# Optimization experiments

Hardware: AMD Instinct MI355X
Metric: run time of the kernel (lower is better)

Reference implementation:

```python
import jax, jax.numpy as jnp
import numpy as np

N, E = 50000, 800000
IN_DIM, H0, H1, OUT_DIM = 64, 64, 64, 8
NUM_RELS, NUM_BASES = 16, 8


def setup_inputs() -> dict:
    key = jax.random.key(0)
    ks = jax.random.split(key, 20)
    features = jax.random.normal(ks[0], (N, IN_DIM), dtype=jnp.float32)
    etypes = jax.random.randint(ks[1], (E,), 0, NUM_RELS)
    src = jax.random.randint(ks[2], (E,), 0, N)
    dst = jax.random.randint(ks[3], (E,), 0, N)
    # degree normalization 1/in_degree(dst), as DGL stores in g.edata['norm']
    deg = jax.ops.segment_sum(jnp.ones((E,), jnp.float32), dst, num_segments=N)
    norm = (1.0 / jnp.maximum(deg, 1.0))[dst][:, None]  # [E,1]

    def glorot(k, shape):
        fan_in, fan_out = shape[-2], shape[-1]
        lim = jnp.sqrt(6.0 / (fan_in + fan_out)).astype(jnp.float32)
        return jax.random.uniform(k, shape, jnp.float32, -lim, lim)

    dims = [(IN_DIM, H0), (H0, H1), (H1, OUT_DIM)]
    inp = {"features": features, "norm": norm}
    for i, (di, do) in enumerate(dims):
        inp[f"basis{i}"] = glorot(ks[4 + 4 * i], (NUM_BASES, di, do))
        inp[f"comp{i}"] = glorot(ks[5 + 4 * i], (NUM_RELS, NUM_BASES))
        inp[f"loop{i}"] = glorot(ks[6 + 4 * i], (di, do))
        inp[f"bias{i}"] = jnp.zeros((do,), jnp.float32)
    inp["etypes"] = etypes
    inp["src"] = src
    inp["dst"] = dst
    return inp


def rel_graph_conv(h, basis, comp, loop_w, bias, etypes, src, dst, norm, act):
    # basis-decomposed relation weights: [R, din, dout]
    W = jnp.einsum('rb,bio->rio', comp, basis)
    # transform every node under every relation: [N, R, dout]
    h_trans = jnp.einsum('ni,rio->nro', h, W)
    # per-edge gather of (src node, edge relation), degree-normalized
    msg = h_trans[src, etypes] * norm  # [E, dout]
    agg = jax.ops.segment_sum(msg, dst, num_segments=h.shape[0])  # [N, dout]
    out = agg + h @ loop_w + bias  # self-loop + bias (DGL defaults)
    return act(out)


def reference(features, norm, basis0, comp0, loop0, bias0, basis1, comp1, loop1,
              bias1, basis2, comp2, loop2, bias2, etypes, src, dst):
    lrelu = lambda x: jax.nn.leaky_relu(x, negative_slope=0.01)
    h = rel_graph_conv(features, basis0, comp0, loop0, bias0, etypes, src, dst, norm, lrelu)
    h = rel_graph_conv(h, basis1, comp1, loop1, bias1, etypes, src, dst, norm, lrelu)
    h = rel_graph_conv(h, basis2, comp2, loop2, bias2, etypes, src, dst, norm, jax.nn.relu)
    return h
```

## Files before the change

kernel.cpp:

```cpp
#include <hip/hip_runtime.h>

#define NN 50000
#define NE 800000
#define CAP 64
#define KC 72
#define RNG 6250
#define EPB 2047

typedef __bf16 bf16x8 __attribute__((ext_vector_type(8)));
typedef float f32x4 __attribute__((ext_vector_type(4)));
typedef float f32x2 __attribute__((ext_vector_type(2)));
typedef unsigned short ushort;
typedef unsigned int uint;

__device__ inline ushort f2bf(float x) {
  uint u = __builtin_bit_cast(uint, x);
  u += 0x7FFF + ((u >> 16) & 1);
  return (ushort)(u >> 16);
}
__device__ inline float bf2f(ushort u) {
  return __builtin_bit_cast(float, (uint)u << 16);
}


__device__ inline void wprep_body(const float* __restrict__ basis,
                                  const float* __restrict__ loopw,
                                  ushort* __restrict__ W2, int DOUT, int NCOLS,
                                  int idx) {
  int total = KC * NCOLS * 8;
  if (idx >= total) return;
  int j = idx & 7;
  int n = (idx >> 3) % NCOLS;
  int kc = idx / (8 * NCOLS);
  int k = kc * 8 + j;
  float v = 0.f;
  if (n < DOUT) v = (k < 512) ? basis[k * DOUT + n] : loopw[(k - 512) * DOUT + n];
  W2[((size_t)kc * NCOLS + n) * 8 + j] = f2bf(v);
}

__global__ __launch_bounds__(256) void build_kernel(
    const int* __restrict__ dstv, const int* __restrict__ srcv,
    const int* __restrict__ etv, int* __restrict__ cursor, int* __restrict__ pk,
    const float* __restrict__ f, ushort* __restrict__ fb,
    const float* __restrict__ b0, const float* __restrict__ l0, ushort* __restrict__ W0,
    const float* __restrict__ b1, const float* __restrict__ l1, ushort* __restrict__ W1,
    const float* __restrict__ b2, const float* __restrict__ l2, ushort* __restrict__ W2,
    const float* __restrict__ c0, const float* __restrict__ c1,
    const float* __restrict__ c2, float* __restrict__ cp) {
  int blk = blockIdx.x;
  int tid = threadIdx.x;
  if (blk < 3128) {
    int sel = blk & 7;
    int sub = blk >> 3;
    int lo = sel * RNG;
    int start = sub * EPB;
    for (int t = tid; t < EPB; t += 256) {
      int i = start + t;
      if (i >= NE) break;
      int d = dstv[i];
      if ((uint)(d - lo) < (uint)RNG) {
        int p = atomicAdd(&cursor[d], 1);
        if (p < CAP) pk[d * CAP + p] = (etv[i] << 16) | srcv[i];
      }
    }
  } else if (blk < 6253) {
    int i = (blk - 3128) * 256 + tid;
    if (i < NN * 16) {
      float4 v = ((const float4*)f)[i];
      ushort4 u;
      u.x = f2bf(v.x); u.y = f2bf(v.y); u.z = f2bf(v.z); u.w = f2bf(v.w);
      ((ushort4*)fb)[i] = u;
    }
  } else if (blk < 6397) {
    wprep_body(b0, l0, W0, 64, 64, (blk - 6253) * 256 + tid);
  } else if (blk < 6541) {
    wprep_body(b1, l1, W1, 64, 64, (blk - 6397) * 256 + tid);
  } else if (blk < 6577) {
    wprep_body(b2, l2, W2, 8, 16, (blk - 6541) * 256 + tid);
  } else {
    int idx = (blk - 6577) * 256 + tid;
    if (idx < 408) {
      int l = idx / 136, k = idx % 136;
      const float* src = (l == 0) ? c0 : ((l == 1) ? c1 : c2);
      cp[idx] = (k < 128) ? src[k] : 0.f;
    }
  }
}


template <int DOUT, int NCOLS, bool OBF>
__global__ __launch_bounds__(1024, 8) void layer_kernel(
    const ushort* __restrict__ hb,
    const float* __restrict__ cpad,
    const int* __restrict__ degv,
    const int* __restrict__ pk,
    const ushort* __restrict__ W2,
    const float* __restrict__ bias,
    void* __restrict__ outp,
    float slope)
{
  __shared__ ushort X[KC][16][8];
  int tid = threadIdx.x;
  int wave = tid >> 6;
  int lane = tid & 63;
  int dbase = blockIdx.x * 16;
  int d = __builtin_amdgcn_readfirstlane(dbase + wave);

  int deg = degv[d];
  int dw = deg > CAP ? CAP : deg;
  const int4* p4 = (const int4*)(pk + (size_t)d * CAP);

  f32x2 acc2[4] = {{0.f, 0.f}, {0.f, 0.f}, {0.f, 0.f}, {0.f, 0.f}};
  for (int base = 0; base < dw; base += 8) {
    int qg = base >> 3;
    int4 e0 = p4[qg * 2];
    int4 e1 = p4[qg * 2 + 1];
    int pe[8] = {e0.x, e0.y, e0.z, e0.w, e1.x, e1.y, e1.z, e1.w};
    float hv[8];
    int ps[8];
#pragma unroll
    for (int i = 0; i < 8; ++i) {
      int pr = __builtin_amdgcn_readfirstlane(pe[i]);
      ps[i] = (base + i < dw) ? pr : (16 << 16);
      hv[i] = bf2f(hb[(size_t)(ps[i] & 0xFFFF) * 64 + lane]);
    }
#pragma unroll
    for (int i = 0; i < 8; ++i) {
      const f32x2* c2 = (const f32x2*)(cpad + (ps[i] >> 16) * 8);
      f32x2 h2 = {hv[i], hv[i]};
#pragma unroll
      for (int j = 0; j < 4; ++j)
        acc2[j] = __builtin_elementwise_fma(c2[j], h2, acc2[j]);
    }
  }

  float inv = 1.0f / (float)(deg > 1 ? deg : 1);
  int jj = lane & 7;
  int csub = lane >> 3;
#pragma unroll
  for (int b = 0; b < 8; ++b) {
    float v = ((b & 1) ? acc2[b >> 1].y : acc2[b >> 1].x) * inv;
    X[b * 8 + csub][wave ^ csub][jj] = f2bf(v);
  }
  X[64 + csub][wave ^ csub][jj] = hb[(size_t)d * 64 + lane];
  __syncthreads();

  if (wave < (DOUT == 64 ? 4 : 1)) {
    int q = lane >> 4;
    int r = lane & 15;
    f32x4 accd = {0.f, 0.f, 0.f, 0.f};
#pragma unroll
    for (int ks = 0; ks < 18; ++ks) {
      int kc = ks * 4 + q;
      bf16x8 bfrag = *(const bf16x8*)&X[kc][r ^ (kc & 7)][0];
      bf16x8 afrag = *(const bf16x8*)(W2 + ((size_t)kc * NCOLS + wave * 16 + r) * 8);
      accd = __builtin_amdgcn_mfma_f32_16x16x32_bf16(afrag, bfrag, accd, 0, 0, 0);
    }
    int m = dbase + r;
    int nb = wave * 16 + q * 4;
    if (nb < DOUT) {
      float4 bv = *(const float4*)(bias + nb);
      float v0 = accd[0] + bv.x;
      float v1 = accd[1] + bv.y;
      float v2 = accd[2] + bv.z;
      float v3 = accd[3] + bv.w;
      v0 = v0 > 0.f ? v0 : slope * v0;
      v1 = v1 > 0.f ? v1 : slope * v1;
      v2 = v2 > 0.f ? v2 : slope * v2;
      v3 = v3 > 0.f ? v3 : slope * v3;
      if (OBF) {
        ushort4 u;
        u.x = f2bf(v0); u.y = f2bf(v1); u.z = f2bf(v2); u.w = f2bf(v3);
        *(ushort4*)((ushort*)outp + (size_t)m * DOUT + nb) = u;
      } else {
        *(float4*)((float*)outp + (size_t)m * DOUT + nb) = float4{v0, v1, v2, v3};
      }
    }
  }
}


extern "C" void kernel_launch(void* const* d_in, const int* in_sizes, int n_in,
                              void* d_out, int out_size, void* d_ws, size_t ws_size,
                              hipStream_t stream) {
  const float* features = (const float*)d_in[0];
  const float* basis0   = (const float*)d_in[2];
  const float* comp0    = (const float*)d_in[3];
  const float* loop0    = (const float*)d_in[4];
  const float* bias0    = (const float*)d_in[5];
  const float* basis1   = (const float*)d_in[6];
  const float* comp1    = (const float*)d_in[7];
  const float* loop1    = (const float*)d_in[8];
  const float* bias1    = (const float*)d_in[9];
  const float* basis2   = (const float*)d_in[10];
  const float* comp2    = (const float*)d_in[11];
  const float* loop2    = (const float*)d_in[12];
  const float* bias2    = (const float*)d_in[13];
  const int* etypes     = (const int*)d_in[14];
  const int* srcv       = (const int*)d_in[15];
  const int* dstv       = (const int*)d_in[16];

  char* ws = (char*)d_ws;
  size_t off = 0;
  auto alloc = [&](size_t bytes) {
    void* p = ws + off;
    off += (bytes + 255) & ~(size_t)255;
    return p;
  };
  int* cnt      = (int*)alloc(NN * sizeof(int));
  int* pk       = (int*)alloc((size_t)NN * CAP * sizeof(int));
  ushort* W2_0  = (ushort*)alloc((size_t)KC * 64 * 8 * sizeof(ushort));
  ushort* W2_1  = (ushort*)alloc((size_t)KC * 64 * 8 * sizeof(ushort));
  ushort* W2_2  = (ushort*)alloc((size_t)KC * 16 * 8 * sizeof(ushort));
  float* cpad   = (float*)alloc(3 * 136 * sizeof(float));
  ushort* fbf   = (ushort*)alloc((size_t)NN * 64 * sizeof(ushort));
  ushort* hA    = (ushort*)alloc((size_t)NN * 64 * sizeof(ushort));
  ushort* hB    = (ushort*)alloc((size_t)NN * 64 * sizeof(ushort));

  hipMemsetAsync(cnt, 0, NN * sizeof(int), stream);
  build_kernel<<<6579, 256, 0, stream>>>(dstv, srcv, etypes, cnt, pk,
                                         features, fbf,
                                         basis0, loop0, W2_0,
                                         basis1, loop1, W2_1,
                                         basis2, loop2, W2_2,
                                         comp0, comp1, comp2, cpad);

  layer_kernel<64, 64, true><<<3125, 1024, 0, stream>>>(
      fbf, cpad + 0 * 136, cnt, pk, W2_0, bias0, hA, 0.01f);
  layer_kernel<64, 64, true><<<3125, 1024, 0, stream>>>(
      hA, cpad + 1 * 136, cnt, pk, W2_1, bias1, hB, 0.01f);
  layer_kernel<8, 16, false><<<3125, 1024, 0, stream>>>(
      hB, cpad + 2 * 136, cnt, pk, W2_2, bias2, d_out, 0.0f);
}
```

Before: 169.7 us.

## Use 256-thread blocks with each wave aggregating four destination nodes

The layer kernel drops from 1024 to 256 threads per block, and each of the 4 waves now processes 4 destination nodes in sequence instead of one node per wave. The gather loop is rewritten to handle edges in groups of 4, software-prefetching the next packed int4 and doing scalar FMAs into 8 accumulators, with a scalar tail for leftover edges. The aim is cheaper block scheduling and fewer idle waves during the MFMA phase. The cost is that each wave now walks four edge lists serially, which exposes more gather latency per wave and leaves fewer loads in flight than the previous 8-wide unrolled batches.

```diff
diff --git a/kernel.cpp b/kernel.cpp
--- a/kernel.cpp
+++ b/kernel.cpp
@@ -9,7 +9,6 @@
 
 typedef __bf16 bf16x8 __attribute__((ext_vector_type(8)));
 typedef float f32x4 __attribute__((ext_vector_type(4)));
-typedef float f32x2 __attribute__((ext_vector_type(2)));
 typedef unsigned short ushort;
 typedef unsigned int uint;
 
@@ -89,7 +88,7 @@
 
 
 template <int DOUT, int NCOLS, bool OBF>
-__global__ __launch_bounds__(1024, 8) void layer_kernel(
+__global__ __launch_bounds__(256, 8) void layer_kernel(
     const ushort* __restrict__ hb,
     const float* __restrict__ cpad,
     const int* __restrict__ degv,
@@ -103,46 +102,70 @@
   int tid = threadIdx.x;
   int wave = tid >> 6;
   int lane = tid & 63;
-  int dbase = blockIdx.x * 16;
-  int d = __builtin_amdgcn_readfirstlane(dbase + wave);
-
-  int deg = degv[d];
-  int dw = deg > CAP ? CAP : deg;
-  const int4* p4 = (const int4*)(pk + (size_t)d * CAP);
-
-  f32x2 acc2[4] = {{0.f, 0.f}, {0.f, 0.f}, {0.f, 0.f}, {0.f, 0.f}};
-  for (int base = 0; base < dw; base += 8) {
-    int qg = base >> 3;
-    int4 e0 = p4[qg * 2];
-    int4 e1 = p4[qg * 2 + 1];
-    int pe[8] = {e0.x, e0.y, e0.z, e0.w, e1.x, e1.y, e1.z, e1.w};
-    float hv[8];
-    int ps[8];
-#pragma unroll
-    for (int i = 0; i < 8; ++i) {
-      int pr = __builtin_amdgcn_readfirstlane(pe[i]);
-      ps[i] = (base + i < dw) ? pr : (16 << 16);
-      hv[i] = bf2f(hb[(size_t)(ps[i] & 0xFFFF) * 64 + lane]);
-    }
-#pragma unroll
-    for (int i = 0; i < 8; ++i) {
-      const f32x2* c2 = (const f32x2*)(cpad + (ps[i] >> 16) * 8);
-      f32x2 h2 = {hv[i], hv[i]};
-#pragma unroll
-      for (int j = 0; j < 4; ++j)
-        acc2[j] = __builtin_elementwise_fma(c2[j], h2, acc2[j]);
-    }
-  }
-
-  float inv = 1.0f / (float)(deg > 1 ? deg : 1);
   int jj = lane & 7;
   int csub = lane >> 3;
-#pragma unroll
-  for (int b = 0; b < 8; ++b) {
-    float v = ((b & 1) ? acc2[b >> 1].y : acc2[b >> 1].x) * inv;
-    X[b * 8 + csub][wave ^ csub][jj] = f2bf(v);
+  int dbase = blockIdx.x * 16;
+
+  for (int t = 0; t < 4; ++t) {
+    int dl = wave * 4 + t;
+    int d = __builtin_amdgcn_readfirstlane(dbase + dl);
+    int deg = degv[d];
+    int dw = deg > CAP ? CAP : deg;
+    const int* pb = pk + (size_t)d * CAP;
+    const int4* p4 = (const int4*)pb;
+    int ng = dw >> 2;
+
+    float acc[8] = {0.f, 0.f, 0.f, 0.f, 0.f, 0.f, 0.f, 0.f};
+    if (ng > 0) {
+      int4 pv = p4[0];
+      for (int g = 0; g < ng; ++g) {
+        int4 nv = pv;
+        if (g + 1 < ng) nv = p4[g + 1];
+        {
+          int pe = __builtin_amdgcn_readfirstlane(pv.x);
+          float hv = bf2f(hb[(size_t)(pe & 0xFFFF) * 64 + lane]);
+          const float* c = cpad + (pe >> 16) * 8;
+#pragma unroll
+          for (int b = 0; b < 8; ++b) acc[b] = fmaf(c[b], hv, acc[b]);
+        }
+        {
+          int pe = __builtin_amdgcn_readfirstlane(pv.y);
+          float hv = bf2f(hb[(size_t)(pe & 0xFFFF) * 64 + lane]);
+          const float* c = cpad + (pe >> 16) * 8;
+#pragma unroll
+          for (int b = 0; b < 8; ++b) acc[b] = fmaf(c[b], hv, acc[b]);
+        }
+        {
+          int pe = __builtin_amdgcn_readfirstlane(pv.z);
+          float hv = bf2f(hb[(size_t)(pe & 0xFFFF) * 64 + lane]);
+          const float* c = cpad + (pe >> 16) * 8;
+#pragma unroll
+          for (int b = 0; b < 8; ++b) acc[b] = fmaf(c[b], hv, acc[b]);
+        }
+        {
+          int pe = __builtin_amdgcn_readfirstlane(pv.w);
+          float hv = bf2f(hb[(size_t)(pe & 0xFFFF) * 64 + lane]);
+          const float* c = cpad + (pe >> 16) * 8;
+#pragma unroll
+          for (int b = 0; b < 8; ++b) acc[b] = fmaf(c[b], hv, acc[b]);
+        }
+        pv = nv;
+      }
+    }
+    for (int j = dw & ~3; j < dw; ++j) {
+      int pe = __builtin_amdgcn_readfirstlane(pb[j]);
+      float hv = bf2f(hb[(size_t)(pe & 0xFFFF) * 64 + lane]);
+      const float* c = cpad + (pe >> 16) * 8;
+#pragma unroll
+      for (int b = 0; b < 8; ++b) acc[b] = fmaf(c[b], hv, acc[b]);
+    }
+
+    float inv = 1.0f / (float)(deg > 1 ? deg : 1);
+#pragma unroll
+    for (int b = 0; b < 8; ++b)
+      X[b * 8 + csub][dl ^ csub][jj] = f2bf(acc[b] * inv);
+    X[64 + csub][dl ^ csub][jj] = hb[(size_t)d * 64 + lane];
   }
-  X[64 + csub][wave ^ csub][jj] = hb[(size_t)d * 64 + lane];
   __syncthreads();
 
   if (wave < (DOUT == 64 ? 4 : 1)) {
@@ -225,10 +248,10 @@
                                          basis2, loop2, W2_2,
                                          comp0, comp1, comp2, cpad);
 
-  layer_kernel<64, 64, true><<<3125, 1024, 0, stream>>>(
+  layer_kernel<64, 64, true><<<3125, 256, 0, stream>>>(
       fbf, cpad + 0 * 136, cnt, pk, W2_0, bias0, hA, 0.01f);
-  layer_kernel<64, 64, true><<<3125, 1024, 0, stream>>>(
+  layer_kernel<64, 64, true><<<3125, 256, 0, stream>>>(
       hA, cpad + 1 * 136, cnt, pk, W2_1, bias1, hB, 0.01f);
-  layer_kernel<8, 16, false><<<3125, 1024, 0, stream>>>(
+  layer_kernel<8, 16, false><<<3125, 256, 0, stream>>>(
       hB, cpad + 2 * 136, cnt, pk, W2_2, bias2, d_out, 0.0f);
 }
```

Result: faster. 158.7 us (-6.5%).
